# Performance work log

Hardware: AMD Instinct MI355X
Metric: run time of the kernel (lower is better)

The kernel has to match this reference:

```python
import jax, jax.numpy as jnp
import numpy as np

PI = np.pi
WIN = (8, 8)
N = WIN[0] * WIN[1]          # 64 tokens per window
NUM_HEADS = 8
DIM = 256
HEAD_DIM = DIM // NUM_HEADS  # 32
P = 4                        # Fourier series order (hardcoded in module)
W_RES = 64                   # input_resolution[1]
SCALE = HEAD_DIM ** -0.5
B_ = 1024                    # num_windows * batch


def _azimuth():
    # relative_coords[:, :, 1] from the torch module: relative column offsets
    ch = np.arange(WIN[0])
    cw = np.arange(WIN[1])
    gh, gw = np.meshgrid(ch, cw, indexing='ij')
    cf = np.stack([gh.ravel(), gw.ravel()])          # (2, N)
    rel = cf[:, :, None] - cf[:, None, :]            # (2, N, N)
    return jnp.asarray(rel[1], dtype=jnp.float32)    # (N, N)


def setup_inputs() -> dict:
    key = jax.random.key(0)
    ks = jax.random.split(key, 12)
    std = 0.02
    return {
        'x': jax.random.normal(ks[0], (B_, N, DIM), dtype=jnp.float32),
        'D': jax.random.uniform(ks[1], (B_, N), dtype=jnp.float32),
        'a_p': std * jax.random.normal(ks[2], (P + 1, NUM_HEADS), dtype=jnp.float32),
        'b_p': std * jax.random.normal(ks[3], (P, NUM_HEADS), dtype=jnp.float32),
        'a_r': std * jax.random.normal(ks[4], (P + 1, NUM_HEADS), dtype=jnp.float32),
        'b_r': std * jax.random.normal(ks[5], (P, NUM_HEADS), dtype=jnp.float32),
        'qkv_w': std * jax.random.normal(ks[6], (3 * DIM, DIM), dtype=jnp.float32),
        'qkv_b': jnp.zeros((3 * DIM,), dtype=jnp.float32),
        'proj_w': std * jax.random.normal(ks[7], (DIM, DIM), dtype=jnp.float32),
        'proj_b': jnp.zeros((DIM,), dtype=jnp.float32),
    }


def reference(x, D, a_p, b_p, a_r, b_r, qkv_w, qkv_b, proj_w, proj_b):
    B, n, C = x.shape

    # ---- azimuth Fourier bias: A_phi, shape (H, N, N) ----
    az = _azimuth() * (2.0 * PI / W_RES)                       # (N, N)
    ii = jnp.arange(1, P + 1, dtype=x.dtype)[:, None, None]    # (P, 1, 1)
    cosP = jnp.cos(ii * az)                                    # (P, N, N)
    sinP = jnp.sin(ii * az)
    A_phi = (jnp.einsum('ph,pij->hij', a_p[1:], cosP)
             + jnp.einsum('ph,pij->hij', b_p, sinP)) / P + a_p[0][:, None, None]

    # ---- radius Fourier bias: A_r, shape (B, N, N, H); rad[b,i,j] = D[b,j] - D[b,i] ----
    rad = D[:, None, :] - D[:, :, None]                        # (B, N, N)
    r_max = 2.0                                                # module overwrites r_max = 2
    A_r = jnp.zeros(rad.shape + (NUM_HEADS,), dtype=x.dtype)
    for i in range(1, P + 1):
        arg = rad * (2.0 * PI * i / r_max)
        A_r = A_r + jnp.cos(arg)[..., None] * a_r[i] + jnp.sin(arg)[..., None] * b_r[i - 1]
    A_r = A_r / P + a_r[0]                                     # (B, N, N, H)

    # ---- attention ----
    qkv = (x @ qkv_w.T + qkv_b).reshape(B, n, 3, NUM_HEADS, HEAD_DIM)
    qkv = qkv.transpose(2, 0, 3, 1, 4)                         # (3, B, H, N, hd)
    q, k, v = qkv[0], qkv[1], qkv[2]
    attn = jnp.einsum('bhid,bhjd->bhij', q * SCALE, k)
    attn = attn + A_phi[None] + A_r.transpose(0, 3, 1, 2)
    attn = jax.nn.softmax(attn, axis=-1)
    out = jnp.einsum('bhij,bhjd->bhid', attn, v)
    out = out.transpose(0, 2, 1, 3).reshape(B, n, C)
    return out @ proj_w.T + proj_b
```

## Files before the change

kernel.cpp:

```cpp
#include <hip/hip_runtime.h>
#include <hip/hip_bf16.h>


using short8  = __attribute__((ext_vector_type(8))) short;
using floatx4 = __attribute__((ext_vector_type(4))) float;

#define PI_F    3.14159265358979323846f
#define SCALE_F 0.17677669529663687f

__global__ void prep_kernel(const float* __restrict__ qw,
                            const float* __restrict__ pw,
                            __hip_bfloat16* __restrict__ dst) {
  int g = blockIdx.x * 256 + threadIdx.x;
  const float4* src;
  __hip_bfloat16* d;
  if (g < 49152) { src = (const float4*)qw + g; d = dst + g * 4; }
  else { int g2 = g - 49152; src = (const float4*)pw + g2; d = dst + 196608 + g2 * 4; }
  float4 v = *src;
  d[0] = __float2bfloat16(v.x);
  d[1] = __float2bfloat16(v.y);
  d[2] = __float2bfloat16(v.z);
  d[3] = __float2bfloat16(v.w);
}

__device__ __forceinline__ void fourier_feats(float dv, int col, float* f) {
  float s1, c1; __sincosf(PI_F * dv, &s1, &c1);
  float c2 = c1*c1 - s1*s1, s2 = 2.f*s1*c1;
  float c3 = c2*c1 - s2*s1, s3 = s2*c1 + c2*s1;
  float c4 = c2*c2 - s2*s2, s4 = 2.f*s2*c2;
  float sa1, ca1; __sincosf((2.f * PI_F / 64.f) * (float)col, &sa1, &ca1);
  float ca2 = ca1*ca1 - sa1*sa1, sa2 = 2.f*sa1*ca1;
  float ca3 = ca2*ca1 - sa2*sa1, sa3 = sa2*ca1 + ca2*sa1;
  float ca4 = ca2*ca2 - sa2*sa2, sa4 = 2.f*sa2*ca2;
  f[0]=c1;  f[1]=c2;  f[2]=c3;  f[3]=c4;
  f[4]=s1;  f[5]=s2;  f[6]=s3;  f[7]=s4;
  f[8]=ca1; f[9]=ca2; f[10]=ca3; f[11]=ca4;
  f[12]=sa1; f[13]=sa2; f[14]=sa3; f[15]=sa4;
}

__global__ __launch_bounds__(512, 2) void fused_kernel(
    const float* __restrict__ x, const float* __restrict__ D,
    const float* __restrict__ a_p, const float* __restrict__ b_p,
    const float* __restrict__ a_r, const float* __restrict__ b_r,
    const __hip_bfloat16* __restrict__ wq, const float* __restrict__ qkv_b,
    const __hip_bfloat16* __restrict__ pwb, const float* __restrict__ pb,
    float* __restrict__ out)
{
  constexpr int LDX = 264, LDQ = 264, LDK = 264, LDQf = 40, LDKm = 136,
                LDVt = 72, LDP = 72, LDO = 264;
  __shared__ __align__(16) __hip_bfloat16 sScr[64 * 264];
  __shared__ __align__(16) __hip_bfloat16 sQ  [64 * 264];
  __shared__ __align__(16) __hip_bfloat16 sK  [64 * 264];
  __shared__ __align__(16) __hip_bfloat16 sQf [64 * 40];
  __shared__ __align__(16) __hip_bfloat16 sKm [64 * 136];
  __shared__ __align__(16) __hip_bfloat16 sVt [256 * 72];

  const int tid = threadIdx.x;
  const int lane = tid & 63, w = tid >> 6;
  const int laneN = lane & 15, laneQ = lane >> 4;
  const int b = blockIdx.x;
  const floatx4 fzero = {0.f, 0.f, 0.f, 0.f};
  const short8 zero8 = {0, 0, 0, 0, 0, 0, 0, 0};

  const float4* xg = (const float4*)(x + (size_t)b * 16384);
  #pragma unroll
  for (int it = 0; it < 8; ++it) {
    int g = tid + it * 512;
    float4 v = xg[g];
    int t = g >> 6, c = (g & 63) * 4;
    __hip_bfloat16* p = &sScr[t * LDX + c];
    p[0] = __float2bfloat16(v.x); p[1] = __float2bfloat16(v.y);
    p[2] = __float2bfloat16(v.z); p[3] = __float2bfloat16(v.w);
  }
  if (tid < 64) {
    float f[16];
    fourier_feats(D[b * 64 + tid], tid & 7, f);
    #pragma unroll
    for (int i = 0; i < 16; ++i) sQf[tid * LDQf + i] = __float2bfloat16(f[i]);
    #pragma unroll
    for (int i = 16; i < 32; ++i) sQf[tid * LDQf + i] = __float2bfloat16(0.f);
  }
  __syncthreads();

  {
    int t = tid >> 3, hh = tid & 7;
    float f[16];
    fourier_feats(D[b * 64 + t], t & 7, f);
    #pragma unroll
    for (int p = 0; p < 4; ++p) {
      float ar = a_r[(p + 1) * 8 + hh], br = b_r[p * 8 + hh];
      float ap = a_p[(p + 1) * 8 + hh], bp = b_p[p * 8 + hh];
      float cr = f[p], sr = f[4 + p], ca = f[8 + p], sa = f[12 + p];
      sKm[t * LDKm + hh * 16 +  0 + p] = __float2bfloat16((ar * cr + br * sr) * 0.25f);
      sKm[t * LDKm + hh * 16 +  4 + p] = __float2bfloat16((ar * sr - br * cr) * 0.25f);
      sKm[t * LDKm + hh * 16 +  8 + p] = __float2bfloat16((ap * ca - bp * sa) * 0.25f);
      sKm[t * LDKm + hh * 16 + 12 + p] = __float2bfloat16((ap * sa + bp * ca) * 0.25f);
    }
  }

  short8 afq[4][8];
  #pragma unroll
  for (int mt = 0; mt < 4; ++mt)
    #pragma unroll
    for (int kk = 0; kk < 8; ++kk)
      afq[mt][kk] = *(const short8*)&sScr[(mt * 16 + laneN) * LDX + kk * 32 + laneQ * 8];

  #pragma unroll
  for (int ni = 0; ni < 6; ++ni) {
    int col0 = (w * 6 + ni) * 16;
    float bias = qkv_b[col0 + laneN];
    short8 bq[8];
    #pragma unroll
    for (int kk = 0; kk < 8; ++kk)
      bq[kk] = *(const short8*)&wq[(size_t)(col0 + laneN) * 256 + kk * 32 + laneQ * 8];
    floatx4 acc[4] = {fzero, fzero, fzero, fzero};
    #pragma unroll
    for (int kk = 0; kk < 8; ++kk)
      #pragma unroll
      for (int mt = 0; mt < 4; ++mt)
        acc[mt] = __builtin_amdgcn_mfma_f32_16x16x32_bf16(afq[mt][kk], bq[kk], acc[mt], 0, 0, 0);
    if (col0 < 256) {
      #pragma unroll
      for (int mt = 0; mt < 4; ++mt)
        #pragma unroll
        for (int r = 0; r < 4; ++r)
          sQ[(mt * 16 + laneQ * 4 + r) * LDQ + col0 + laneN] =
              __float2bfloat16((acc[mt][r] + bias) * SCALE_F);
    } else if (col0 < 512) {
      #pragma unroll
      for (int mt = 0; mt < 4; ++mt)
        #pragma unroll
        for (int r = 0; r < 4; ++r)
          sK[(mt * 16 + laneQ * 4 + r) * LDK + (col0 - 256) + laneN] =
              __float2bfloat16(acc[mt][r] + bias);
    } else {
      int vd = col0 - 512 + laneN;
      #pragma unroll
      for (int mt = 0; mt < 4; ++mt)
        #pragma unroll
        for (int r = 0; r < 4; ++r)
          sVt[vd * LDVt + (mt * 16 + laneQ * 4 + r)] = __float2bfloat16(acc[mt][r] + bias);
    }
  }
  __syncthreads();

  const int h = w;
  short8 qf0[4], qf1[4], kf0[4], kf1[4];
  #pragma unroll
  for (int mt = 0; mt < 4; ++mt) {
    qf0[mt] = *(const short8*)&sQ[(mt * 16 + laneN) * LDQ + h * 32 + laneQ * 8];
    qf1[mt] = *(const short8*)&sQf[(mt * 16 + laneN) * LDQf + laneQ * 8];
  }
  #pragma unroll
  for (int nt = 0; nt < 4; ++nt) {
    kf0[nt] = *(const short8*)&sK[(nt * 16 + laneN) * LDK + h * 32 + laneQ * 8];
    short8 km = *(const short8*)&sKm[(nt * 16 + laneN) * LDKm + h * 16 + (laneQ & 1) * 8];
    kf1[nt] = (laneQ < 2) ? km : zero8;
  }
  floatx4 s[4][4];
  #pragma unroll
  for (int mt = 0; mt < 4; ++mt)
    #pragma unroll
    for (int nt = 0; nt < 4; ++nt) {
      s[mt][nt] = __builtin_amdgcn_mfma_f32_16x16x32_bf16(qf0[mt], kf0[nt], fzero, 0, 0, 0);
      s[mt][nt] = __builtin_amdgcn_mfma_f32_16x16x32_bf16(qf1[mt], kf1[nt], s[mt][nt], 0, 0, 0);
    }

  short8 vb[2][2];
  #pragma unroll
  for (int ont = 0; ont < 2; ++ont)
    #pragma unroll
    for (int kk = 0; kk < 2; ++kk)
      vb[ont][kk] = *(const short8*)&sVt[(h * 32 + ont * 16 + laneN) * LDVt + kk * 32 + laneQ * 8];

  floatx4 oacc[4][2];
  __hip_bfloat16* Pw = &sScr[w * 16 * LDP];
  #pragma unroll
  for (int mt = 0; mt < 4; ++mt) {
    #pragma unroll
    for (int r = 0; r < 4; ++r) {
      float mx = fmaxf(fmaxf(s[mt][0][r], s[mt][1][r]), fmaxf(s[mt][2][r], s[mt][3][r]));
      mx = fmaxf(mx, __shfl_xor(mx, 1));
      mx = fmaxf(mx, __shfl_xor(mx, 2));
      mx = fmaxf(mx, __shfl_xor(mx, 4));
      mx = fmaxf(mx, __shfl_xor(mx, 8));
      float e0 = __expf(s[mt][0][r] - mx), e1 = __expf(s[mt][1][r] - mx);
      float e2 = __expf(s[mt][2][r] - mx), e3 = __expf(s[mt][3][r] - mx);
      float sum = e0 + e1 + e2 + e3;
      sum += __shfl_xor(sum, 1);
      sum += __shfl_xor(sum, 2);
      sum += __shfl_xor(sum, 4);
      sum += __shfl_xor(sum, 8);
      float inv = __builtin_amdgcn_rcpf(sum);
      int pr = laneQ * 4 + r;
      Pw[pr * LDP +  0 + laneN] = __float2bfloat16(e0 * inv);
      Pw[pr * LDP + 16 + laneN] = __float2bfloat16(e1 * inv);
      Pw[pr * LDP + 32 + laneN] = __float2bfloat16(e2 * inv);
      Pw[pr * LDP + 48 + laneN] = __float2bfloat16(e3 * inv);
    }
    short8 pf0 = *(const short8*)&Pw[laneN * LDP + laneQ * 8];
    short8 pf1 = *(const short8*)&Pw[laneN * LDP + 32 + laneQ * 8];
    #pragma unroll
    for (int ont = 0; ont < 2; ++ont) {
      oacc[mt][ont] = __builtin_amdgcn_mfma_f32_16x16x32_bf16(pf0, vb[ont][0], fzero, 0, 0, 0);
      oacc[mt][ont] = __builtin_amdgcn_mfma_f32_16x16x32_bf16(pf1, vb[ont][1], oacc[mt][ont], 0, 0, 0);
    }
  }
  __syncthreads();

  #pragma unroll
  for (int mt = 0; mt < 4; ++mt)
    #pragma unroll
    for (int ont = 0; ont < 2; ++ont)
      #pragma unroll
      for (int r = 0; r < 4; ++r)
        sScr[(mt * 16 + laneQ * 4 + r) * LDO + h * 32 + ont * 16 + laneN] =
            __float2bfloat16(oacc[mt][ont][r]);
  __syncthreads();

  const int col0 = w * 32;
  floatx4 pacc[4][2];
  #pragma unroll
  for (int mt = 0; mt < 4; ++mt) { pacc[mt][0] = fzero; pacc[mt][1] = fzero; }
  #pragma unroll
  for (int kk = 0; kk < 8; ++kk) {
    short8 pa[4], pbf[2];
    #pragma unroll
    for (int mt = 0; mt < 4; ++mt)
      pa[mt] = *(const short8*)&sScr[(mt * 16 + laneN) * LDO + kk * 32 + laneQ * 8];
    #pragma unroll
    for (int n2 = 0; n2 < 2; ++n2)
      pbf[n2] = *(const short8*)&pwb[(size_t)(col0 + n2 * 16 + laneN) * 256 + kk * 32 + laneQ * 8];
    #pragma unroll
    for (int mt = 0; mt < 4; ++mt)
      #pragma unroll
      for (int n2 = 0; n2 < 2; ++n2)
        pacc[mt][n2] = __builtin_amdgcn_mfma_f32_16x16x32_bf16(pa[mt], pbf[n2], pacc[mt][n2], 0, 0, 0);
  }
  float bias0 = pb[col0 + laneN], bias1 = pb[col0 + 16 + laneN];
  float* og = out + (size_t)b * 16384;
  #pragma unroll
  for (int mt = 0; mt < 4; ++mt)
    #pragma unroll
    for (int n2 = 0; n2 < 2; ++n2)
      #pragma unroll
      for (int r = 0; r < 4; ++r)
        og[(mt * 16 + laneQ * 4 + r) * 256 + col0 + n2 * 16 + laneN] =
            pacc[mt][n2][r] + (n2 ? bias1 : bias0);
}

extern "C" void kernel_launch(void* const* d_in, const int* in_sizes, int n_in,
                              void* d_out, int out_size, void* d_ws, size_t ws_size,
                              hipStream_t stream) {
  const float* x      = (const float*)d_in[0];
  const float* D      = (const float*)d_in[1];
  const float* a_p    = (const float*)d_in[2];
  const float* b_p    = (const float*)d_in[3];
  const float* a_r    = (const float*)d_in[4];
  const float* b_r    = (const float*)d_in[5];
  const float* qkv_w  = (const float*)d_in[6];
  const float* qkv_b  = (const float*)d_in[7];
  const float* proj_w = (const float*)d_in[8];
  const float* proj_b = (const float*)d_in[9];

  __hip_bfloat16* wq  = (__hip_bfloat16*)d_ws;
  __hip_bfloat16* pwb = wq + 196608;
  float* out = (float*)d_out;

  prep_kernel<<<256, 256, 0, stream>>>(qkv_w, proj_w, wq);
  fused_kernel<<<1024, 512, 0, stream>>>(x, D, a_p, b_p, a_r, b_r, wq, qkv_b,
                                         pwb, proj_b, out);
}
```

Measured before the change: 211.0 us.

## Restructure window attention kernel: per-wave head processing with swizzled LDS and register-resident Q/K/V

Rewrites the fused window-attention kernel to use 256 threads. Each wave computes Q, K and V for two heads directly in registers and keeps the per-head pipeline wave-local, so the large Q/K/V shared buffers and most block-wide barriers go away. LDS layouts switch from padded strides to XOR swizzles, V is transposed with cross-lane shuffles instead of LDS, and outputs are written as float4. Shared memory use drops sharply, which may allow more blocks per CU, at the cost of more register pressure and fewer waves per block.

```diff
diff --git a/kernel.cpp b/kernel.cpp
--- a/kernel.cpp
+++ b/kernel.cpp
@@ -3,10 +3,23 @@
 
 
 using short8  = __attribute__((ext_vector_type(8))) short;
+using short4v = __attribute__((ext_vector_type(4))) short;
 using floatx4 = __attribute__((ext_vector_type(4))) float;
+using uint4v  = __attribute__((ext_vector_type(4))) unsigned int;
 
 #define PI_F    3.14159265358979323846f
 #define SCALE_F 0.17677669529663687f
+
+__device__ __forceinline__ short bfs(float x) {
+  __hip_bfloat16 h = __float2bfloat16(x);
+  return __builtin_bit_cast(short, h);
+}
+
+__device__ __forceinline__ unsigned pk2(float a, float b) {
+  unsigned lo = (unsigned short)bfs(a);
+  unsigned hi = (unsigned short)bfs(b);
+  return lo | (hi << 16);
+}
 
 __global__ void prep_kernel(const float* __restrict__ qw,
                             const float* __restrict__ pw,
@@ -38,7 +51,7 @@
   f[12]=sa1; f[13]=sa2; f[14]=sa3; f[15]=sa4;
 }
 
-__global__ __launch_bounds__(512, 2) void fused_kernel(
+__global__ __launch_bounds__(256, 2) void win_kernel(
     const float* __restrict__ x, const float* __restrict__ D,
     const float* __restrict__ a_p, const float* __restrict__ b_p,
     const float* __restrict__ a_r, const float* __restrict__ b_r,
@@ -46,14 +59,9 @@
     const __hip_bfloat16* __restrict__ pwb, const float* __restrict__ pb,
     float* __restrict__ out)
 {
-  constexpr int LDX = 264, LDQ = 264, LDK = 264, LDQf = 40, LDKm = 136,
-                LDVt = 72, LDP = 72, LDO = 264;
-  __shared__ __align__(16) __hip_bfloat16 sScr[64 * 264];
-  __shared__ __align__(16) __hip_bfloat16 sQ  [64 * 264];
-  __shared__ __align__(16) __hip_bfloat16 sK  [64 * 264];
-  __shared__ __align__(16) __hip_bfloat16 sQf [64 * 40];
-  __shared__ __align__(16) __hip_bfloat16 sKm [64 * 136];
-  __shared__ __align__(16) __hip_bfloat16 sVt [256 * 72];
+  __shared__ __align__(16) __hip_bfloat16 sX  [64 * 256];
+  __shared__ __align__(16) __hip_bfloat16 sStr[4 * 4096];
+  __shared__ __align__(16) __hip_bfloat16 sQf [64 * 32];
 
   const int tid = threadIdx.x;
   const int lane = tid & 63, w = tid >> 6;
@@ -62,191 +70,289 @@
   const floatx4 fzero = {0.f, 0.f, 0.f, 0.f};
   const short8 zero8 = {0, 0, 0, 0, 0, 0, 0, 0};
 
+  char* xb = (char*)sX;
+  char* sb = (char*)sStr + w * 8192;
+
+  float f[16];
+  fourier_feats(D[b * 64 + lane], lane & 7, f);
+
   const float4* xg = (const float4*)(x + (size_t)b * 16384);
   #pragma unroll
-  for (int it = 0; it < 8; ++it) {
-    int g = tid + it * 512;
+  for (int it = 0; it < 16; ++it) {
+    int g = tid + it * 256;
     float4 v = xg[g];
-    int t = g >> 6, c = (g & 63) * 4;
-    __hip_bfloat16* p = &sScr[t * LDX + c];
-    p[0] = __float2bfloat16(v.x); p[1] = __float2bfloat16(v.y);
-    p[2] = __float2bfloat16(v.z); p[3] = __float2bfloat16(v.w);
+    int t = g >> 6;
+    int off = (t * 512 + (g & 63) * 8) ^ ((t & 7) << 4);
+    short4v pk = { bfs(v.x), bfs(v.y), bfs(v.z), bfs(v.w) };
+    *(short4v*)(xb + off) = pk;
   }
   if (tid < 64) {
-    float f[16];
-    fourier_feats(D[b * 64 + tid], tid & 7, f);
-    #pragma unroll
-    for (int i = 0; i < 16; ++i) sQf[tid * LDQf + i] = __float2bfloat16(f[i]);
-    #pragma unroll
-    for (int i = 16; i < 32; ++i) sQf[tid * LDQf + i] = __float2bfloat16(0.f);
+    int t = tid;
+    uint4v q0 = { pk2(f[0],f[1]),  pk2(f[2],f[3]),  pk2(f[4],f[5]),   pk2(f[6],f[7]) };
+    uint4v q1 = { pk2(f[8],f[9]),  pk2(f[10],f[11]),pk2(f[12],f[13]), pk2(f[14],f[15]) };
+    uint4v zz = { 0u, 0u, 0u, 0u };
+    char* qb = (char*)sQf;
+    *(uint4v*)(qb + ((t * 64 +  0) ^ ((t & 3) << 4))) = q0;
+    *(uint4v*)(qb + ((t * 64 + 16) ^ ((t & 3) << 4))) = q1;
+    *(uint4v*)(qb + ((t * 64 + 32) ^ ((t & 3) << 4))) = zz;
+    *(uint4v*)(qb + ((t * 64 + 48) ^ ((t & 3) << 4))) = zz;
   }
   __syncthreads();
 
-  {
-    int t = tid >> 3, hh = tid & 7;
-    float f[16];
-    fourier_feats(D[b * 64 + t], t & 7, f);
-    #pragma unroll
-    for (int p = 0; p < 4; ++p) {
-      float ar = a_r[(p + 1) * 8 + hh], br = b_r[p * 8 + hh];
-      float ap = a_p[(p + 1) * 8 + hh], bp = b_p[p * 8 + hh];
-      float cr = f[p], sr = f[4 + p], ca = f[8 + p], sa = f[12 + p];
-      sKm[t * LDKm + hh * 16 +  0 + p] = __float2bfloat16((ar * cr + br * sr) * 0.25f);
-      sKm[t * LDKm + hh * 16 +  4 + p] = __float2bfloat16((ar * sr - br * cr) * 0.25f);
-      sKm[t * LDKm + hh * 16 +  8 + p] = __float2bfloat16((ap * ca - bp * sa) * 0.25f);
-      sKm[t * LDKm + hh * 16 + 12 + p] = __float2bfloat16((ap * sa + bp * ca) * 0.25f);
-    }
-  }
-
-  short8 afq[4][8];
+  for (int hi = 0; hi < 2; ++hi) {
+    const int hh = w + hi * 4;
+
+    floatx4 Qa[4][2], Ka[4][2], Va[4][2];
+    #pragma unroll
+    for (int mt = 0; mt < 4; ++mt)
+      #pragma unroll
+      for (int ont = 0; ont < 2; ++ont) { Qa[mt][ont]=fzero; Ka[mt][ont]=fzero; Va[mt][ont]=fzero; }
+
+    const __hip_bfloat16* wqQ = wq + (size_t)(      hh*32 + laneN) * 256 + laneQ * 8;
+    const __hip_bfloat16* wqK = wq + (size_t)(256 + hh*32 + laneN) * 256 + laneQ * 8;
+    const __hip_bfloat16* wqV = wq + (size_t)(512 + hh*32 + laneN) * 256 + laneQ * 8;
+
+    #pragma unroll
+    for (int kk = 0; kk < 8; ++kk) {
+      short8 a4[4];
+      #pragma unroll
+      for (int mt = 0; mt < 4; ++mt) {
+        int off = ((mt*16 + laneN) * 512 + kk*64 + laneQ*16) ^ ((laneN & 7) << 4);
+        a4[mt] = *(const short8*)(xb + off);
+      }
+      #pragma unroll
+      for (int ont = 0; ont < 2; ++ont) {
+        short8 fq = *(const short8*)(wqQ + (size_t)ont*16*256 + kk*32);
+        short8 fk = *(const short8*)(wqK + (size_t)ont*16*256 + kk*32);
+        short8 fv = *(const short8*)(wqV + (size_t)ont*16*256 + kk*32);
+        #pragma unroll
+        for (int mt = 0; mt < 4; ++mt) {
+          Qa[mt][ont] = __builtin_amdgcn_mfma_f32_16x16x32_bf16(fq, a4[mt], Qa[mt][ont], 0, 0, 0);
+          Ka[mt][ont] = __builtin_amdgcn_mfma_f32_16x16x32_bf16(fk, a4[mt], Ka[mt][ont], 0, 0, 0);
+          Va[mt][ont] = __builtin_amdgcn_mfma_f32_16x16x32_bf16(a4[mt], fv, Va[mt][ont], 0, 0, 0);
+        }
+      }
+    }
+
+    {
+      float4 b0 = *(const float4*)&qkv_b[hh*32 +      laneQ*4];
+      float4 b1 = *(const float4*)&qkv_b[hh*32 + 16 + laneQ*4];
+      float qba[2][4] = {{b0.x,b0.y,b0.z,b0.w},{b1.x,b1.y,b1.z,b1.w}};
+      #pragma unroll
+      for (int mt = 0; mt < 4; ++mt)
+        #pragma unroll
+        for (int ont = 0; ont < 2; ++ont) {
+          short4v pq;
+          #pragma unroll
+          for (int r = 0; r < 4; ++r)
+            pq[r] = bfs((Qa[mt][ont][r] + qba[ont][r]) * SCALE_F);
+          int off = ((mt*16 + laneN) * 64 + ont*32 + laneQ*8) ^ ((laneN & 3) << 4);
+          *(short4v*)(sb + off) = pq;
+        }
+    }
+    short8 qf[4];
+    #pragma unroll
+    for (int ct = 0; ct < 4; ++ct)
+      qf[ct] = *(const short8*)(sb + (((ct*16 + laneN) * 64 + laneQ*16) ^ ((laneN & 3) << 4)));
+
+    {
+      float4 b0 = *(const float4*)&qkv_b[256 + hh*32 +      laneQ*4];
+      float4 b1 = *(const float4*)&qkv_b[256 + hh*32 + 16 + laneQ*4];
+      float kba[2][4] = {{b0.x,b0.y,b0.z,b0.w},{b1.x,b1.y,b1.z,b1.w}};
+      #pragma unroll
+      for (int mt = 0; mt < 4; ++mt)
+        #pragma unroll
+        for (int ont = 0; ont < 2; ++ont) {
+          short4v pk;
+          #pragma unroll
+          for (int r = 0; r < 4; ++r)
+            pk[r] = bfs(Ka[mt][ont][r] + kba[ont][r]);
+          int off = ((mt*16 + laneN) * 64 + ont*32 + laneQ*8) ^ ((laneN & 3) << 4);
+          *(short4v*)(sb + off) = pk;
+        }
+    }
+    short8 kf[4];
+    #pragma unroll
+    for (int rt = 0; rt < 4; ++rt)
+      kf[rt] = *(const short8*)(sb + (((rt*16 + laneN) * 64 + laneQ*16) ^ ((laneN & 3) << 4)));
+
+    {
+      float m0[4], m1[4], m2[4], m3[4];
+      #pragma unroll
+      for (int p = 0; p < 4; ++p) {
+        float ar = a_r[(p+1)*8 + hh], br = b_r[p*8 + hh];
+        float ap = a_p[(p+1)*8 + hh], bp = b_p[p*8 + hh];
+        m0[p] = (ar*f[p]     + br*f[4+p])  * 0.25f;
+        m1[p] = (ar*f[4+p]   - br*f[p])    * 0.25f;
+        m2[p] = (ap*f[8+p]   - bp*f[12+p]) * 0.25f;
+        m3[p] = (ap*f[12+p]  + bp*f[8+p])  * 0.25f;
+      }
+      uint4v k0 = { pk2(m0[0],m0[1]), pk2(m0[2],m0[3]), pk2(m1[0],m1[1]), pk2(m1[2],m1[3]) };
+      uint4v k1 = { pk2(m2[0],m2[1]), pk2(m2[2],m2[3]), pk2(m3[0],m3[1]), pk2(m3[2],m3[3]) };
+      *(uint4v*)(sb + lane * 32)      = k0;
+      *(uint4v*)(sb + lane * 32 + 16) = k1;
+    }
+    short8 kmf[4];
+    #pragma unroll
+    for (int rt = 0; rt < 4; ++rt) {
+      short8 t8 = *(const short8*)(sb + (rt*16 + laneN) * 32 + (laneQ & 1) * 16);
+      kmf[rt] = (laneQ < 2) ? t8 : zero8;
+    }
+    short8 qff[4];
+    #pragma unroll
+    for (int ct = 0; ct < 4; ++ct)
+      qff[ct] = *(const short8*)((char*)sQf + (((ct*16 + laneN) * 64 + laneQ*16) ^ ((laneN & 3) << 4)));
+
+    short8 vf[2][2];
+    {
+      float bv0 = qkv_b[512 + hh*32 +      laneN];
+      float bv1 = qkv_b[512 + hh*32 + 16 + laneN];
+      unsigned pkV[4][2][2];
+      #pragma unroll
+      for (int mt = 0; mt < 4; ++mt)
+        #pragma unroll
+        for (int ont = 0; ont < 2; ++ont) {
+          float bv = ont ? bv1 : bv0;
+          pkV[mt][ont][0] = pk2(Va[mt][ont][0] + bv, Va[mt][ont][1] + bv);
+          pkV[mt][ont][1] = pk2(Va[mt][ont][2] + bv, Va[mt][ont][3] + bv);
+        }
+      int idxLo = laneN + 32 * (laneQ & 1);
+      int idxHi = idxLo + 16;
+      bool hiSel = (laneQ >= 2);
+      #pragma unroll
+      for (int ont = 0; ont < 2; ++ont)
+        #pragma unroll
+        for (int kb = 0; kb < 2; ++kb) {
+          uint4v u;
+          #pragma unroll
+          for (int j = 0; j < 4; ++j) {
+            int idx = (j < 2) ? idxLo : idxHi;
+            unsigned lo = (unsigned)__shfl((int)pkV[2*kb    ][ont][j & 1], idx);
+            unsigned hi = (unsigned)__shfl((int)pkV[2*kb + 1][ont][j & 1], idx);
+            u[j] = hiSel ? hi : lo;
+          }
+          vf[ont][kb] = __builtin_bit_cast(short8, u);
+        }
+    }
+
+    floatx4 S[4][4];
+    #pragma unroll
+    for (int rt = 0; rt < 4; ++rt)
+      #pragma unroll
+      for (int ct = 0; ct < 4; ++ct) {
+        S[rt][ct] = __builtin_amdgcn_mfma_f32_16x16x32_bf16(kf[rt], qf[ct], fzero, 0, 0, 0);
+        S[rt][ct] = __builtin_amdgcn_mfma_f32_16x16x32_bf16(kmf[rt], qff[ct], S[rt][ct], 0, 0, 0);
+      }
+
+    float inv4[4];
+    #pragma unroll
+    for (int ct = 0; ct < 4; ++ct) {
+      float mx = S[0][ct][0];
+      #pragma unroll
+      for (int rt = 0; rt < 4; ++rt)
+        #pragma unroll
+        for (int r = 0; r < 4; ++r)
+          mx = fmaxf(mx, S[rt][ct][r]);
+      mx = fmaxf(mx, __shfl_xor(mx, 16));
+      mx = fmaxf(mx, __shfl_xor(mx, 32));
+      float sum = 0.f;
+      #pragma unroll
+      for (int rt = 0; rt < 4; ++rt)
+        #pragma unroll
+        for (int r = 0; r < 4; ++r) {
+          S[rt][ct][r] = __expf(S[rt][ct][r] - mx);
+          sum += S[rt][ct][r];
+        }
+      sum += __shfl_xor(sum, 16);
+      sum += __shfl_xor(sum, 32);
+      inv4[ct] = __builtin_amdgcn_rcpf(sum);
+    }
+
+    floatx4 Oa[2][4];
+    #pragma unroll
+    for (int cp = 0; cp < 2; ++cp) {
+      #pragma unroll
+      for (int cc = 0; cc < 2; ++cc) {
+        int ct = cp * 2 + cc;
+        #pragma unroll
+        for (int rt = 0; rt < 4; ++rt) {
+          short4v pp;
+          #pragma unroll
+          for (int r = 0; r < 4; ++r)
+            pp[r] = bfs(S[rt][ct][r] * inv4[ct]);
+          int off = ((cc*16 + laneN) * 128 + rt*32 + laneQ*8) ^ ((laneN & 7) << 4);
+          *(short4v*)(sb + off) = pp;
+        }
+      }
+      #pragma unroll
+      for (int cc = 0; cc < 2; ++cc) {
+        int ct = cp * 2 + cc;
+        short8 pf0 = *(const short8*)(sb + (((cc*16 + laneN) * 128 +  0 + laneQ*16) ^ ((laneN & 7) << 4)));
+        short8 pf1 = *(const short8*)(sb + (((cc*16 + laneN) * 128 + 64 + laneQ*16) ^ ((laneN & 7) << 4)));
+        #pragma unroll
+        for (int ont = 0; ont < 2; ++ont) {
+          Oa[ont][ct] = __builtin_amdgcn_mfma_f32_16x16x32_bf16(vf[ont][0], pf0, fzero, 0, 0, 0);
+          Oa[ont][ct] = __builtin_amdgcn_mfma_f32_16x16x32_bf16(vf[ont][1], pf1, Oa[ont][ct], 0, 0, 0);
+        }
+      }
+    }
+
+    {
+      int obase = hi ? 0 : 4096;
+      #pragma unroll
+      for (int ont = 0; ont < 2; ++ont)
+        #pragma unroll
+        for (int ct = 0; ct < 4; ++ct) {
+          short4v po;
+          #pragma unroll
+          for (int r = 0; r < 4; ++r)
+            po[r] = bfs(Oa[ont][ct][r]);
+          int off = obase + (((ct*16 + laneN) * 64 + ont*32 + laneQ*8) ^ ((laneN & 3) << 4));
+          *(short4v*)(sb + off) = po;
+        }
+    }
+  }
+  __syncthreads();
+
+  floatx4 pacc[4][4];
   #pragma unroll
   for (int mt = 0; mt < 4; ++mt)
     #pragma unroll
-    for (int kk = 0; kk < 8; ++kk)
-      afq[mt][kk] = *(const short8*)&sScr[(mt * 16 + laneN) * LDX + kk * 32 + laneQ * 8];
-
-  #pragma unroll
-  for (int ni = 0; ni < 6; ++ni) {
-    int col0 = (w * 6 + ni) * 16;
-    float bias = qkv_b[col0 + laneN];
-    short8 bq[8];
-    #pragma unroll
-    for (int kk = 0; kk < 8; ++kk)
-      bq[kk] = *(const short8*)&wq[(size_t)(col0 + laneN) * 256 + kk * 32 + laneQ * 8];
-    floatx4 acc[4] = {fzero, fzero, fzero, fzero};
-    #pragma unroll
-    for (int kk = 0; kk < 8; ++kk)
-      #pragma unroll
-      for (int mt = 0; mt < 4; ++mt)
-        acc[mt] = __builtin_amdgcn_mfma_f32_16x16x32_bf16(afq[mt][kk], bq[kk], acc[mt], 0, 0, 0);
-    if (col0 < 256) {
-      #pragma unroll
-      for (int mt = 0; mt < 4; ++mt)
-        #pragma unroll
-        for (int r = 0; r < 4; ++r)
-          sQ[(mt * 16 + laneQ * 4 + r) * LDQ + col0 + laneN] =
-              __float2bfloat16((acc[mt][r] + bias) * SCALE_F);
-    } else if (col0 < 512) {
-      #pragma unroll
-      for (int mt = 0; mt < 4; ++mt)
-        #pragma unroll
-        for (int r = 0; r < 4; ++r)
-          sK[(mt * 16 + laneQ * 4 + r) * LDK + (col0 - 256) + laneN] =
-              __float2bfloat16(acc[mt][r] + bias);
-    } else {
-      int vd = col0 - 512 + laneN;
-      #pragma unroll
-      for (int mt = 0; mt < 4; ++mt)
-        #pragma unroll
-        for (int r = 0; r < 4; ++r)
-          sVt[vd * LDVt + (mt * 16 + laneQ * 4 + r)] = __float2bfloat16(acc[mt][r] + bias);
-    }
-  }
-  __syncthreads();
-
-  const int h = w;
-  short8 qf0[4], qf1[4], kf0[4], kf1[4];
-  #pragma unroll
-  for (int mt = 0; mt < 4; ++mt) {
-    qf0[mt] = *(const short8*)&sQ[(mt * 16 + laneN) * LDQ + h * 32 + laneQ * 8];
-    qf1[mt] = *(const short8*)&sQf[(mt * 16 + laneN) * LDQf + laneQ * 8];
-  }
-  #pragma unroll
-  for (int nt = 0; nt < 4; ++nt) {
-    kf0[nt] = *(const short8*)&sK[(nt * 16 + laneN) * LDK + h * 32 + laneQ * 8];
-    short8 km = *(const short8*)&sKm[(nt * 16 + laneN) * LDKm + h * 16 + (laneQ & 1) * 8];
-    kf1[nt] = (laneQ < 2) ? km : zero8;
-  }
-  floatx4 s[4][4];
-  #pragma unroll
-  for (int mt = 0; mt < 4; ++mt)
-    #pragma unroll
-    for (int nt = 0; nt < 4; ++nt) {
-      s[mt][nt] = __builtin_amdgcn_mfma_f32_16x16x32_bf16(qf0[mt], kf0[nt], fzero, 0, 0, 0);
-      s[mt][nt] = __builtin_amdgcn_mfma_f32_16x16x32_bf16(qf1[mt], kf1[nt], s[mt][nt], 0, 0, 0);
-    }
-
-  short8 vb[2][2];
-  #pragma unroll
-  for (int ont = 0; ont < 2; ++ont)
-    #pragma unroll
-    for (int kk = 0; kk < 2; ++kk)
-      vb[ont][kk] = *(const short8*)&sVt[(h * 32 + ont * 16 + laneN) * LDVt + kk * 32 + laneQ * 8];
-
-  floatx4 oacc[4][2];
-  __hip_bfloat16* Pw = &sScr[w * 16 * LDP];
-  #pragma unroll
-  for (int mt = 0; mt < 4; ++mt) {
-    #pragma unroll
-    for (int r = 0; r < 4; ++r) {
-      float mx = fmaxf(fmaxf(s[mt][0][r], s[mt][1][r]), fmaxf(s[mt][2][r], s[mt][3][r]));
-      mx = fmaxf(mx, __shfl_xor(mx, 1));
-      mx = fmaxf(mx, __shfl_xor(mx, 2));
-      mx = fmaxf(mx, __shfl_xor(mx, 4));
-      mx = fmaxf(mx, __shfl_xor(mx, 8));
-      float e0 = __expf(s[mt][0][r] - mx), e1 = __expf(s[mt][1][r] - mx);
-      float e2 = __expf(s[mt][2][r] - mx), e3 = __expf(s[mt][3][r] - mx);
-      float sum = e0 + e1 + e2 + e3;
-      sum += __shfl_xor(sum, 1);
-      sum += __shfl_xor(sum, 2);
-      sum += __shfl_xor(sum, 4);
-      sum += __shfl_xor(sum, 8);
-      float inv = __builtin_amdgcn_rcpf(sum);
-      int pr = laneQ * 4 + r;
-      Pw[pr * LDP +  0 + laneN] = __float2bfloat16(e0 * inv);
-      Pw[pr * LDP + 16 + laneN] = __float2bfloat16(e1 * inv);
-      Pw[pr * LDP + 32 + laneN] = __float2bfloat16(e2 * inv);
-      Pw[pr * LDP + 48 + laneN] = __float2bfloat16(e3 * inv);
-    }
-    short8 pf0 = *(const short8*)&Pw[laneN * LDP + laneQ * 8];
-    short8 pf1 = *(const short8*)&Pw[laneN * LDP + 32 + laneQ * 8];
-    #pragma unroll
-    for (int ont = 0; ont < 2; ++ont) {
-      oacc[mt][ont] = __builtin_amdgcn_mfma_f32_16x16x32_bf16(pf0, vb[ont][0], fzero, 0, 0, 0);
-      oacc[mt][ont] = __builtin_amdgcn_mfma_f32_16x16x32_bf16(pf1, vb[ont][1], oacc[mt][ont], 0, 0, 0);
-    }
-  }
-  __syncthreads();
-
-  #pragma unroll
-  for (int mt = 0; mt < 4; ++mt)
-    #pragma unroll
-    for (int ont = 0; ont < 2; ++ont)
-      #pragma unroll
-      for (int r = 0; r < 4; ++r)
-        sScr[(mt * 16 + laneQ * 4 + r) * LDO + h * 32 + ont * 16 + laneN] =
-            __float2bfloat16(oacc[mt][ont][r]);
-  __syncthreads();
-
-  const int col0 = w * 32;
-  floatx4 pacc[4][2];
-  #pragma unroll
-  for (int mt = 0; mt < 4; ++mt) { pacc[mt][0] = fzero; pacc[mt][1] = fzero; }
+    for (int n = 0; n < 4; ++n) pacc[mt][n] = fzero;
+
+  const __hip_bfloat16* pwr = pwb + (size_t)(w*64 + laneN) * 256 + laneQ * 8;
   #pragma unroll
   for (int kk = 0; kk < 8; ++kk) {
-    short8 pa[4], pbf[2];
+    char* ob = (char*)sStr + (kk & 3) * 8192 + ((kk < 4) ? 4096 : 0);
+    short8 pa[4];
     #pragma unroll
     for (int mt = 0; mt < 4; ++mt)
-      pa[mt] = *(const short8*)&sScr[(mt * 16 + laneN) * LDO + kk * 32 + laneQ * 8];
-    #pragma unroll
-    for (int n2 = 0; n2 < 2; ++n2)
-      pbf[n2] = *(const short8*)&pwb[(size_t)(col0 + n2 * 16 + laneN) * 256 + kk * 32 + laneQ * 8];
+      pa[mt] = *(const short8*)(ob + (((mt*16 + laneN) * 64 + laneQ*16) ^ ((laneN & 3) << 4)));
+    short8 pw4[4];
+    #pragma unroll
+    for (int n = 0; n < 4; ++n)
+      pw4[n] = *(const short8*)(pwr + (size_t)n*16*256 + kk*32);
     #pragma unroll
     for (int mt = 0; mt < 4; ++mt)
       #pragma unroll
-      for (int n2 = 0; n2 < 2; ++n2)
-        pacc[mt][n2] = __builtin_amdgcn_mfma_f32_16x16x32_bf16(pa[mt], pbf[n2], pacc[mt][n2], 0, 0, 0);
-  }
-  float bias0 = pb[col0 + laneN], bias1 = pb[col0 + 16 + laneN];
+      for (int n = 0; n < 4; ++n)
+        pacc[mt][n] = __builtin_amdgcn_mfma_f32_16x16x32_bf16(pw4[n], pa[mt], pacc[mt][n], 0, 0, 0);
+  }
+
   float* og = out + (size_t)b * 16384;
   #pragma unroll
-  for (int mt = 0; mt < 4; ++mt)
-    #pragma unroll
-    for (int n2 = 0; n2 < 2; ++n2)
-      #pragma unroll
-      for (int r = 0; r < 4; ++r)
-        og[(mt * 16 + laneQ * 4 + r) * 256 + col0 + n2 * 16 + laneN] =
-            pacc[mt][n2][r] + (n2 ? bias1 : bias0);
+  for (int n = 0; n < 4; ++n) {
+    float4 b4 = *(const float4*)&pb[w*64 + n*16 + laneQ*4];
+    #pragma unroll
+    for (int mt = 0; mt < 4; ++mt) {
+      float4 o4;
+      o4.x = pacc[mt][n][0] + b4.x;
+      o4.y = pacc[mt][n][1] + b4.y;
+      o4.z = pacc[mt][n][2] + b4.z;
+      o4.w = pacc[mt][n][3] + b4.w;
+      *(float4*)&og[(mt*16 + laneN) * 256 + w*64 + n*16 + laneQ*4] = o4;
+    }
+  }
 }
 
 extern "C" void kernel_launch(void* const* d_in, const int* in_sizes, int n_in,
@@ -268,6 +374,6 @@
   float* out = (float*)d_out;
 
   prep_kernel<<<256, 256, 0, stream>>>(qkv_w, proj_w, wq);
-  fused_kernel<<<1024, 512, 0, stream>>>(x, D, a_p, b_p, a_r, b_r, wq, qkv_b,
-                                         pwb, proj_b, out);
-}
+  win_kernel<<<1024, 256, 0, stream>>>(x, D, a_p, b_p, a_r, b_r, wq, qkv_b,
+                                       pwb, proj_b, out);
+}
```

Measured after the change: 268.3 us. 27.1% more time.
